# Kernel optimization log

Hardware: AMD Instinct MI355X
Metric: run time of the kernel (lower is better)

Reference implementation:

```python
import jax, jax.numpy as jnp
import numpy as np

L, T, D, H, NC = 4, 2, 128, 8, 7
DH = D // H
DFF = 4 * D
EPS = 1e-5


def _ln(x, w, b):
    m = jnp.mean(x, axis=-1, keepdims=True)
    v = jnp.mean((x - m) ** 2, axis=-1, keepdims=True)
    return (x - m) / jnp.sqrt(v + EPS) * w + b


def setup_inputs() -> dict:
    key = jax.random.key(0)
    ks = jax.random.split(key, 16)
    s = 0.02
    inp = {
        "x": jax.random.normal(ks[0], (65536, 1, 2 * D), dtype=jnp.float32),
        "token_proj_w": jax.random.normal(ks[1], (T * D, T * D), dtype=jnp.float32) * s,
        "token_proj_b": jnp.zeros((T * D,), jnp.float32),
        "pos_emb": jax.random.normal(ks[2], (1, T, D), dtype=jnp.float32),
        "qkv_w": jax.random.normal(ks[3], (L, 3 * D, D), dtype=jnp.float32) * s,
        "qkv_b": jnp.zeros((L, 3 * D), jnp.float32),
        "out_w": jax.random.normal(ks[4], (L, D, D), dtype=jnp.float32) * s,
        "out_b": jnp.zeros((L, D), jnp.float32),
        "ln1_w": jnp.ones((L, D), jnp.float32),
        "ln1_b": jnp.zeros((L, D), jnp.float32),
        "ff1_w": jax.random.normal(ks[5], (L, DFF, D), dtype=jnp.float32) * s,
        "ff1_b": jnp.zeros((L, DFF), jnp.float32),
        "ff2_w": jax.random.normal(ks[6], (L, D, DFF), dtype=jnp.float32) * s,
        "ff2_b": jnp.zeros((L, D), jnp.float32),
        "ln2_w": jnp.ones((L, D), jnp.float32),
        "ln2_b": jnp.zeros((L, D), jnp.float32),
        "lnf_w": jnp.ones((D,), jnp.float32),
        "lnf_b": jnp.zeros((D,), jnp.float32),
        "cls_ln_w": jnp.ones((D,), jnp.float32),
        "cls_ln_b": jnp.zeros((D,), jnp.float32),
        "cls_w": jax.random.normal(ks[7], (NC, D), dtype=jnp.float32) * s,
        "cls_b": jnp.zeros((NC,), jnp.float32),
    }
    return inp


def _forward(x, token_proj_w, token_proj_b, pos_emb, qkv_w, qkv_b, out_w, out_b,
             ln1_w, ln1_b, ff1_w, ff1_b, ff2_w, ff2_b, ln2_w, ln2_b,
             lnf_w, lnf_b, cls_ln_w, cls_ln_b, cls_w, cls_b):
    x = jnp.squeeze(x, 1)                                  # [B, 256]
    B = x.shape[0]
    tok = x @ token_proj_w.T + token_proj_b                # [B, 256]
    tok = tok.reshape(B, T, D) + pos_emb                   # [B, 2, 128]
    scale = 1.0 / jnp.sqrt(jnp.float32(DH))
    for i in range(L):
        # --- self-attention (post-norm, as in nn.TransformerEncoderLayer) ---
        qkv = jnp.einsum('btd,ed->bte', tok, qkv_w[i]) + qkv_b[i]   # [B,T,3D]
        q, k, v = jnp.split(qkv, 3, axis=-1)
        q = q.reshape(B, T, H, DH)
        k = k.reshape(B, T, H, DH)
        v = v.reshape(B, T, H, DH)
        scores = jnp.einsum('bqhd,bkhd->bhqk', q, k) * scale
        attn = jax.nn.softmax(scores, axis=-1)
        o = jnp.einsum('bhqk,bkhd->bqhd', attn, v).reshape(B, T, D)
        o = jnp.einsum('btd,ed->bte', o, out_w[i]) + out_b[i]
        tok = _ln(tok + o, ln1_w[i], ln1_b[i])
        # --- FFN ---
        h = jnp.einsum('btd,fd->btf', tok, ff1_w[i]) + ff1_b[i]
        h = jax.nn.gelu(h, approximate=False)
        h = jnp.einsum('btf,df->btd', h, ff2_w[i]) + ff2_b[i]
        tok = _ln(tok + h, ln2_w[i], ln2_b[i])
    tok = _ln(tok, lnf_w, lnf_b)                           # final encoder norm
    pooled = jnp.mean(tok, axis=1)                         # [B, D]
    out = _ln(pooled, cls_ln_w, cls_ln_b)
    out = jax.nn.gelu(out, approximate=False)
    return out @ cls_w.T + cls_b                           # [B, 7]


def reference(x, token_proj_w, token_proj_b, pos_emb, qkv_w, qkv_b, out_w, out_b,
              ln1_w, ln1_b, ff1_w, ff1_b, ff2_w, ff2_b, ln2_w, ln2_b,
              lnf_w, lnf_b, cls_ln_w, cls_ln_b, cls_w, cls_b):
    return _forward(x, token_proj_w, token_proj_b, pos_emb, qkv_w, qkv_b, out_w, out_b,
                    ln1_w, ln1_b, ff1_w, ff1_b, ff2_w, ff2_b, ln2_w, ln2_b,
                    lnf_w, lnf_b, cls_ln_w, cls_ln_b, cls_w, cls_b)
```

## Files before the change

kernel.cpp:

```cpp
#include <hip/hip_runtime.h>


#define DEV static __device__ __forceinline__

typedef __attribute__((ext_vector_type(8))) short short8;
typedef __attribute__((ext_vector_type(4))) float f32x4;

#define BS    32
#define MROWS 64
#define PITCH 136
#define XP    272
#define LEPS  1e-5f

#define OFF_TPW  0
#define OFF_QKVW 65536
#define OFF_OUTW 262144
#define OFF_FF1W 327680
#define OFF_FF2W 589824
#define WS_ELEMS 851968

DEV unsigned short f2b(float f) {
  unsigned u = __float_as_uint(f);
  return (unsigned short)((u + 0x7fffu + ((u >> 16) & 1u)) >> 16);
}
DEV float b2f(unsigned short s) { return __uint_as_float((unsigned)s << 16); }

DEV f32x4 MFMA(short8 a, short8 b, f32x4 c) {
  return __builtin_amdgcn_mfma_f32_16x16x32_bf16(a, b, c, 0, 0, 0);
}

DEV float gelu_f(float x) {
  float u = 0.7978845608028654f * (x + 0.044715f * x * x * x);
  float e = __expf(2.0f * u);
  float t = 1.0f - 2.0f / (e + 1.0f);
  return 0.5f * x * (1.0f + t);
}

DEV short8 ldfrag(const unsigned short* tile, int rowBase, int kk, int lane) {
  return *(const short8*)(tile + (rowBase + (lane & 15)) * PITCH + kk * 32 + (lane >> 4) * 8);
}
DEV short8 ldfragX(const unsigned short* tile, int rowBase, int koff, int lane) {
  return *(const short8*)(tile + (rowBase + (lane & 15)) * XP + koff + (lane >> 4) * 8);
}
DEV short8 ldBg(const unsigned short* __restrict__ base, int pitch, int colBase,
                int koff, int kk, int lane) {
  return *(const short8*)(base + (size_t)(colBase + (lane & 15)) * pitch +
                          koff + kk * 32 + (lane >> 4) * 8);
}

DEV void ln_residual_write(f32x4 (&val)[2][4], const float* __restrict__ w,
                           const float* __restrict__ b, unsigned short* sTok,
                           float* sRedP, float* sRedF, int tid) {
  const int wave = tid >> 6, lane = tid & 63, g = lane >> 4, j = lane & 15;
  float ps[4][4], pq[4][4];
#pragma unroll
  for (int rt = 0; rt < 4; ++rt)
#pragma unroll
    for (int r = 0; r < 4; ++r) {
      float v0 = val[0][rt][r], v1 = val[1][rt][r];
      float s = v0 + v1, q = v0 * v0 + v1 * v1;
#pragma unroll
      for (int m = 1; m < 16; m <<= 1) {
        s += __shfl_xor(s, m, 16);
        q += __shfl_xor(q, m, 16);
      }
      ps[rt][r] = s; pq[rt][r] = q;
    }
  if (j == 0) {
#pragma unroll
    for (int rt = 0; rt < 4; ++rt)
#pragma unroll
      for (int r = 0; r < 4; ++r) {
        int row = rt * 16 + g * 4 + r;
        sRedP[row * 8 + wave * 2]     = ps[rt][r];
        sRedP[row * 8 + wave * 2 + 1] = pq[rt][r];
      }
  }
  __syncthreads();
  if (tid < 64) {
    float s = 0.f, q = 0.f;
#pragma unroll
    for (int wv = 0; wv < 4; ++wv) {
      s += sRedP[tid * 8 + wv * 2];
      q += sRedP[tid * 8 + wv * 2 + 1];
    }
    float mean = s * (1.f / 128.f);
    sRedF[tid * 2]     = mean;
    sRedF[tid * 2 + 1] = rsqrtf(q * (1.f / 128.f) - mean * mean + LEPS);
  }
  __syncthreads();
#pragma unroll
  for (int h = 0; h < 2; ++h) {
    int n = (h * 4 + wave) * 16 + j;
    float wn = w[n], bn = b[n];
#pragma unroll
    for (int rt = 0; rt < 4; ++rt)
#pragma unroll
      for (int r = 0; r < 4; ++r) {
        int row = rt * 16 + g * 4 + r;
        float mean = sRedF[row * 2], rstd = sRedF[row * 2 + 1];
        sTok[row * PITCH + n] = f2b((val[h][rt][r] - mean) * rstd * wn + bn);
      }
  }
  __syncthreads();
}

__global__ __launch_bounds__(256)
void prep_w(const float* __restrict__ tpw, const float* __restrict__ qkvw,
            const float* __restrict__ outw, const float* __restrict__ ff1w,
            const float* __restrict__ ff2w, unsigned short* __restrict__ wsb) {
  int i = blockIdx.x * 256 + threadIdx.x;
  if (i >= WS_ELEMS) return;
  float v;
  if (i < OFF_QKVW)      v = tpw[i - OFF_TPW];
  else if (i < OFF_OUTW) v = qkvw[i - OFF_QKVW];
  else if (i < OFF_FF1W) v = outw[i - OFF_OUTW];
  else if (i < OFF_FF2W) v = ff1w[i - OFF_FF1W];
  else                   v = ff2w[i - OFF_FF2W];
  wsb[i] = f2b(v);
}

__global__ __launch_bounds__(256, 2)
void tx_fused(const float* __restrict__ x, const unsigned short* __restrict__ wsb,
              const float* __restrict__ tpb, const float* __restrict__ pos,
              const float* __restrict__ qkvb, const float* __restrict__ outb,
              const float* __restrict__ ln1w, const float* __restrict__ ln1b,
              const float* __restrict__ ff1b, const float* __restrict__ ff2b,
              const float* __restrict__ ln2w, const float* __restrict__ ln2b,
              const float* __restrict__ lnfw, const float* __restrict__ lnfb,
              const float* __restrict__ clnw, const float* __restrict__ clnb,
              const float* __restrict__ cw, const float* __restrict__ cb,
              float* __restrict__ out) {
  __shared__ __align__(16) unsigned short sTok[MROWS * PITCH];
  __shared__ __align__(16) unsigned short sStage[MROWS * PITCH];
  __shared__ float sRedP[MROWS * 8];
  __shared__ float sRedF[MROWS * 2];

  const int tid  = threadIdx.x;
  const int wave = tid >> 6;
  const int lane = tid & 63;
  const int g = lane >> 4, j = lane & 15;
  const size_t s0 = (size_t)blockIdx.x * BS;

  const unsigned short* tpwB  = wsb + OFF_TPW;
  const unsigned short* qkvwB = wsb + OFF_QKVW;
  const unsigned short* outwB = wsb + OFF_OUTW;
  const unsigned short* ff1wB = wsb + OFF_FF1W;
  const unsigned short* ff2wB = wsb + OFF_FF2W;

  const f32x4 zero4 = {0.f, 0.f, 0.f, 0.f};

  {
#pragma unroll
    for (int it = 0; it < 2; ++it) {
      int idx = it * 256 + tid;
      int r = idx >> 4, s = idx & 15;
      const float4* p = (const float4*)(x + (s0 + r) * 256 + s * 16);
      float4 f0 = p[0], f1 = p[1], f2 = p[2], f3 = p[3];
      short8 lo, hi;
      lo[0] = (short)f2b(f0.x); lo[1] = (short)f2b(f0.y);
      lo[2] = (short)f2b(f0.z); lo[3] = (short)f2b(f0.w);
      lo[4] = (short)f2b(f1.x); lo[5] = (short)f2b(f1.y);
      lo[6] = (short)f2b(f1.z); lo[7] = (short)f2b(f1.w);
      hi[0] = (short)f2b(f2.x); hi[1] = (short)f2b(f2.y);
      hi[2] = (short)f2b(f2.z); hi[3] = (short)f2b(f2.w);
      hi[4] = (short)f2b(f3.x); hi[5] = (short)f2b(f3.y);
      hi[6] = (short)f2b(f3.z); hi[7] = (short)f2b(f3.w);
      *(short8*)(sStage + r * XP + s * 16)     = lo;
      *(short8*)(sStage + r * XP + s * 16 + 8) = hi;
    }
  }
  __syncthreads();

  f32x4 accTP[2][2][2];
#pragma unroll
  for (int nc = 0; nc < 2; ++nc)
#pragma unroll
    for (int h = 0; h < 2; ++h)
#pragma unroll
      for (int rt = 0; rt < 2; ++rt) accTP[nc][h][rt] = zero4;

#pragma unroll
  for (int kc = 0; kc < 2; ++kc)
#pragma unroll
    for (int nc = 0; nc < 2; ++nc)
#pragma unroll
      for (int h = 0; h < 2; ++h) {
        int cb = nc * 128 + (h * 4 + wave) * 16;
        short8 bf[4];
#pragma unroll
        for (int kk = 0; kk < 4; ++kk)
          bf[kk] = ldBg(tpwB, 256, cb, kc * 128, kk, lane);
#pragma unroll
        for (int rt = 0; rt < 2; ++rt)
#pragma unroll
          for (int kk = 0; kk < 4; ++kk)
            accTP[nc][h][rt] = MFMA(ldfragX(sStage, rt * 16, kc * 128 + kk * 32, lane),
                                    bf[kk], accTP[nc][h][rt]);
      }
  __syncthreads();
#pragma unroll
  for (int nc = 0; nc < 2; ++nc)
#pragma unroll
    for (int h = 0; h < 2; ++h) {
      int d = (h * 4 + wave) * 16 + j;
      float bias = tpb[nc * 128 + d] + pos[nc * 128 + d];
#pragma unroll
      for (int rt = 0; rt < 2; ++rt)
#pragma unroll
        for (int r = 0; r < 4; ++r) {
          int sm = rt * 16 + g * 4 + r;
          sTok[(2 * sm + nc) * PITCH + d] = f2b(accTP[nc][h][rt][r] + bias);
        }
    }
  __syncthreads();

  for (int li = 0; li < 4; ++li) {
    const unsigned short* qkvL = qkvwB + (size_t)li * 49152;
    const unsigned short* outL = outwB + (size_t)li * 16384;
    const unsigned short* ff1L = ff1wB + (size_t)li * 65536;
    const unsigned short* ff2L = ff2wB + (size_t)li * 65536;

    short8 aT[4][4];
#pragma unroll
    for (int rt = 0; rt < 4; ++rt)
#pragma unroll
      for (int kk = 0; kk < 4; ++kk) aT[rt][kk] = ldfrag(sTok, rt * 16, kk, lane);

    f32x4 acc[6][4];
#pragma unroll
    for (int a = 0; a < 6; ++a)
#pragma unroll
      for (int rt = 0; rt < 4; ++rt) acc[a][rt] = zero4;

#pragma unroll
    for (int nc = 0; nc < 3; ++nc)
#pragma unroll
      for (int h = 0; h < 2; ++h) {
        int cb = nc * 128 + (h * 4 + wave) * 16;
        short8 bf[4];
#pragma unroll
        for (int kk = 0; kk < 4; ++kk) bf[kk] = ldBg(qkvL, 128, cb, 0, kk, lane);
        int a = nc * 2 + h;
#pragma unroll
        for (int rt = 0; rt < 4; ++rt)
#pragma unroll
          for (int kk = 0; kk < 4; ++kk)
            acc[a][rt] = MFMA(aT[rt][kk], bf[kk], acc[a][rt]);
      }
#pragma unroll
    for (int a = 0; a < 6; ++a) {
      int nc = a >> 1, h = a & 1;
      float bv = qkvb[li * 384 + nc * 128 + (h * 4 + wave) * 16 + j];
#pragma unroll
      for (int rt = 0; rt < 4; ++rt) acc[a][rt] += bv;
    }

#pragma unroll
    for (int hh = 0; hh < 2; ++hh) {
      int head = hh * 4 + wave;
#pragma unroll
      for (int rt = 0; rt < 4; ++rt)
#pragma unroll
        for (int sp = 0; sp < 2; ++sp) {
          int r0 = sp * 2, r1 = r0 + 1;
          float q0 = acc[hh][rt][r0],     q1 = acc[hh][rt][r1];
          float k0 = acc[2 + hh][rt][r0], k1 = acc[2 + hh][rt][r1];
          float s00 = q0 * k0, s01 = q0 * k1, s10 = q1 * k0, s11 = q1 * k1;
#pragma unroll
          for (int m = 1; m < 16; m <<= 1) {
            s00 += __shfl_xor(s00, m, 16);
            s01 += __shfl_xor(s01, m, 16);
            s10 += __shfl_xor(s10, m, 16);
            s11 += __shfl_xor(s11, m, 16);
          }
          s00 *= 0.25f; s01 *= 0.25f; s10 *= 0.25f; s11 *= 0.25f;
          float m0 = fmaxf(s00, s01), m1 = fmaxf(s10, s11);
          float e00 = __expf(s00 - m0), e01 = __expf(s01 - m0);
          float e10 = __expf(s10 - m1), e11 = __expf(s11 - m1);
          float i0 = 1.f / (e00 + e01), i1 = 1.f / (e10 + e11);
          float v0 = acc[4 + hh][rt][r0], v1 = acc[4 + hh][rt][r1];
          float o0 = (e00 * v0 + e01 * v1) * i0;
          float o1 = (e10 * v0 + e11 * v1) * i1;
          int rowb = rt * 16 + g * 4 + r0;
          int col  = head * 16 + j;
          sStage[rowb * PITCH + col]       = f2b(o0);
          sStage[(rowb + 1) * PITCH + col] = f2b(o1);
        }
    }
    __syncthreads();

    short8 aO[4][4];
#pragma unroll
    for (int rt = 0; rt < 4; ++rt)
#pragma unroll
      for (int kk = 0; kk < 4; ++kk) aO[rt][kk] = ldfrag(sStage, rt * 16, kk, lane);

    f32x4 accO[2][4];
#pragma unroll
    for (int h = 0; h < 2; ++h)
#pragma unroll
      for (int rt = 0; rt < 4; ++rt) accO[h][rt] = zero4;
#pragma unroll
    for (int h = 0; h < 2; ++h) {
      int cb = (h * 4 + wave) * 16;
      short8 bf[4];
#pragma unroll
      for (int kk = 0; kk < 4; ++kk) bf[kk] = ldBg(outL, 128, cb, 0, kk, lane);
#pragma unroll
      for (int rt = 0; rt < 4; ++rt)
#pragma unroll
        for (int kk = 0; kk < 4; ++kk)
          accO[h][rt] = MFMA(aO[rt][kk], bf[kk], accO[h][rt]);
    }
#pragma unroll
    for (int h = 0; h < 2; ++h) {
      int n = (h * 4 + wave) * 16 + j;
      float ob = outb[li * 128 + n];
#pragma unroll
      for (int rt = 0; rt < 4; ++rt)
#pragma unroll
        for (int r = 0; r < 4; ++r) {
          int row = rt * 16 + g * 4 + r;
          accO[h][rt][r] += ob + b2f(sTok[row * PITCH + n]);
        }
    }
    ln_residual_write(accO, ln1w + li * 128, ln1b + li * 128, sTok, sRedP, sRedF, tid);

    short8 aF[4][4];
#pragma unroll
    for (int rt = 0; rt < 4; ++rt)
#pragma unroll
      for (int kk = 0; kk < 4; ++kk) aF[rt][kk] = ldfrag(sTok, rt * 16, kk, lane);

    f32x4 accF[2][4];
#pragma unroll
    for (int h = 0; h < 2; ++h)
#pragma unroll
      for (int rt = 0; rt < 4; ++rt) accF[h][rt] = zero4;

    for (int fc = 0; fc < 4; ++fc) {
      f32x4 hacc[2][4];
#pragma unroll
      for (int h = 0; h < 2; ++h)
#pragma unroll
        for (int rt = 0; rt < 4; ++rt) hacc[h][rt] = zero4;
#pragma unroll
      for (int h = 0; h < 2; ++h) {
        int cb = fc * 128 + (h * 4 + wave) * 16;
        short8 bf[4];
#pragma unroll
        for (int kk = 0; kk < 4; ++kk) bf[kk] = ldBg(ff1L, 128, cb, 0, kk, lane);
#pragma unroll
        for (int rt = 0; rt < 4; ++rt)
#pragma unroll
          for (int kk = 0; kk < 4; ++kk)
            hacc[h][rt] = MFMA(aF[rt][kk], bf[kk], hacc[h][rt]);
      }
      __syncthreads();
#pragma unroll
      for (int h = 0; h < 2; ++h) {
        int nl = (h * 4 + wave) * 16 + j;
        float bb = ff1b[li * 512 + fc * 128 + nl];
#pragma unroll
        for (int rt = 0; rt < 4; ++rt)
#pragma unroll
          for (int r = 0; r < 4; ++r) {
            float hv = gelu_f(hacc[h][rt][r] + bb);
            sStage[(rt * 16 + g * 4 + r) * PITCH + nl] = f2b(hv);
          }
      }
      __syncthreads();
      short8 aH[4][4];
#pragma unroll
      for (int rt = 0; rt < 4; ++rt)
#pragma unroll
        for (int kk = 0; kk < 4; ++kk) aH[rt][kk] = ldfrag(sStage, rt * 16, kk, lane);
#pragma unroll
      for (int h = 0; h < 2; ++h) {
        int cb = (h * 4 + wave) * 16;
        short8 bf[4];
#pragma unroll
        for (int kk = 0; kk < 4; ++kk)
          bf[kk] = ldBg(ff2L, 512, cb, fc * 128, kk, lane);
#pragma unroll
        for (int rt = 0; rt < 4; ++rt)
#pragma unroll
          for (int kk = 0; kk < 4; ++kk)
            accF[h][rt] = MFMA(aH[rt][kk], bf[kk], accF[h][rt]);
      }
    }
#pragma unroll
    for (int h = 0; h < 2; ++h) {
      int n = (h * 4 + wave) * 16 + j;
      float fb = ff2b[li * 128 + n];
#pragma unroll
      for (int rt = 0; rt < 4; ++rt)
#pragma unroll
        for (int r = 0; r < 4; ++r) {
          int row = rt * 16 + g * 4 + r;
          accF[h][rt][r] += fb + b2f(sTok[row * PITCH + n]);
        }
    }
    ln_residual_write(accF, ln2w + li * 128, ln2b + li * 128, sTok, sRedP, sRedF, tid);
  }

  {
    int row = tid >> 2, q4 = tid & 3;
    const unsigned short* rp = sTok + row * PITCH + q4 * 32;
    float vb[32];
    float s = 0.f, sq = 0.f;
#pragma unroll
    for (int t8 = 0; t8 < 4; ++t8) {
      short8 v = *(const short8*)(rp + t8 * 8);
#pragma unroll
      for (int e = 0; e < 8; ++e) {
        float f = b2f((unsigned short)v[e]);
        vb[t8 * 8 + e] = f; s += f; sq += f * f;
      }
    }
    s  += __shfl_xor(s, 1, 4);  s  += __shfl_xor(s, 2, 4);
    sq += __shfl_xor(sq, 1, 4); sq += __shfl_xor(sq, 2, 4);
    float mean = s * (1.f / 128.f);
    float rstd = rsqrtf(sq * (1.f / 128.f) - mean * mean + LEPS);
    unsigned short* wp = sTok + row * PITCH + q4 * 32;
#pragma unroll
    for (int c = 0; c < 32; ++c) {
      int col = q4 * 32 + c;
      wp[c] = f2b((vb[c] - mean) * rstd * lnfw[col] + lnfb[col]);
    }
  }
  __syncthreads();
  {
    int sIdx = tid >> 3, oct = tid & 7;
    float pv[16];
    float s = 0.f, sq = 0.f;
#pragma unroll
    for (int t8 = 0; t8 < 2; ++t8) {
      short8 va  = *(const short8*)(sTok + (2 * sIdx) * PITCH + oct * 16 + t8 * 8);
      short8 vb2 = *(const short8*)(sTok + (2 * sIdx + 1) * PITCH + oct * 16 + t8 * 8);
#pragma unroll
      for (int e = 0; e < 8; ++e) {
        float f = 0.5f * (b2f((unsigned short)va[e]) + b2f((unsigned short)vb2[e]));
        pv[t8 * 8 + e] = f; s += f; sq += f * f;
      }
    }
    s  += __shfl_xor(s, 1, 8);  s  += __shfl_xor(s, 2, 8);  s  += __shfl_xor(s, 4, 8);
    sq += __shfl_xor(sq, 1, 8); sq += __shfl_xor(sq, 2, 8); sq += __shfl_xor(sq, 4, 8);
    float mean = s * (1.f / 128.f);
    float rstd = rsqrtf(sq * (1.f / 128.f) - mean * mean + LEPS);
    float gv[16];
#pragma unroll
    for (int c = 0; c < 16; ++c) {
      int col = oct * 16 + c;
      gv[c] = gelu_f((pv[c] - mean) * rstd * clnw[col] + clnb[col]);
    }
#pragma unroll
    for (int cc = 0; cc < 7; ++cc) {
      float p = 0.f;
#pragma unroll
      for (int c = 0; c < 16; ++c) p += gv[c] * cw[cc * 128 + oct * 16 + c];
      p += __shfl_xor(p, 1, 8); p += __shfl_xor(p, 2, 8); p += __shfl_xor(p, 4, 8);
      if (oct == 0) out[(s0 + sIdx) * 7 + cc] = p + cb[cc];
    }
  }
}

extern "C" void kernel_launch(void* const* d_in, const int* in_sizes, int n_in,
                              void* d_out, int out_size, void* d_ws, size_t ws_size,
                              hipStream_t stream) {
  (void)n_in; (void)out_size; (void)ws_size;
  const float* x    = (const float*)d_in[0];
  const float* tpw  = (const float*)d_in[1];
  const float* tpb  = (const float*)d_in[2];
  const float* pos  = (const float*)d_in[3];
  const float* qkvw = (const float*)d_in[4];
  const float* qkvb = (const float*)d_in[5];
  const float* outw = (const float*)d_in[6];
  const float* outb = (const float*)d_in[7];
  const float* ln1w = (const float*)d_in[8];
  const float* ln1b = (const float*)d_in[9];
  const float* ff1w = (const float*)d_in[10];
  const float* ff1b = (const float*)d_in[11];
  const float* ff2w = (const float*)d_in[12];
  const float* ff2b = (const float*)d_in[13];
  const float* ln2w = (const float*)d_in[14];
  const float* ln2b = (const float*)d_in[15];
  const float* lnfw = (const float*)d_in[16];
  const float* lnfb = (const float*)d_in[17];
  const float* clnw = (const float*)d_in[18];
  const float* clnb = (const float*)d_in[19];
  const float* cw   = (const float*)d_in[20];
  const float* cb   = (const float*)d_in[21];
  unsigned short* wsb = (unsigned short*)d_ws;

  int B = in_sizes[0] / 256;

  hipLaunchKernelGGL(prep_w, dim3((WS_ELEMS + 255) / 256), dim3(256), 0, stream,
                     tpw, qkvw, outw, ff1w, ff2w, wsb);
  hipLaunchKernelGGL(tx_fused, dim3(B / BS), dim3(256), 0, stream,
                     x, wsb, tpb, pos, qkvb, outb, ln1w, ln1b, ff1b, ff2b,
                     ln2w, ln2b, lnfw, lnfb, clnw, clnb, cw, cb, (float*)d_out);
}
```

Measured before the change: 719.3 us.

## Prefetch next-stage weight fragments into LDS with async global-to-LDS loads

Adds a per-wave LDS prefetch buffer and uses global_load_lds to fetch the weight fragments of the next GEMM stage (the first QKV slice, out-proj, the first FF1 chunk, FF2 chunks, and the next layer's QKV) while the current stage computes. Each stage then waits on vmcnt and reads its B fragments from LDS instead of issuing blocking global loads right before the MFMAs. This is meant to hide global/L2 weight-load latency. In exchange it adds 32KB of LDS per block, which pressures the two-blocks-per-CU occupancy target. The full vmcnt(0) waits can also serialize against other outstanding loads, and reuse of the buffer relies on ordering between the LDS reads and the next async writes.

```diff
diff --git a/kernel.cpp b/kernel.cpp
--- a/kernel.cpp
+++ b/kernel.cpp
@@ -47,6 +47,27 @@
   return *(const short8*)(base + (size_t)(colBase + (lane & 15)) * pitch +
                           koff + kk * 32 + (lane >> 4) * 8);
 }
+
+DEV void pf_issue(unsigned short* sPF, int wave, int lane,
+                  const unsigned short* __restrict__ base, int pitch,
+                  int ncoff, int koff) {
+#pragma unroll
+  for (int h = 0; h < 2; ++h)
+#pragma unroll
+    for (int kk = 0; kk < 4; ++kk) {
+      int cb = ncoff + (h * 4 + wave) * 16;
+      const unsigned short* src = base + (size_t)(cb + (lane & 15)) * pitch +
+                                  koff + kk * 32 + (lane >> 4) * 8;
+      __builtin_amdgcn_global_load_lds(
+          (const __attribute__((address_space(1))) void*)src,
+          (__attribute__((address_space(3))) void*)(sPF + wave * 4096 + (h * 4 + kk) * 512),
+          16, 0, 0);
+    }
+}
+DEV short8 pf_read(const unsigned short* sPF, int wave, int h, int kk, int lane) {
+  return *(const short8*)(sPF + wave * 4096 + (h * 4 + kk) * 512 + lane * 8);
+}
+#define PF_WAIT() asm volatile("s_waitcnt vmcnt(0)" ::: "memory")
 
 DEV void ln_residual_write(f32x4 (&val)[2][4], const float* __restrict__ w,
                            const float* __restrict__ b, unsigned short* sTok,
@@ -133,6 +154,7 @@
               float* __restrict__ out) {
   __shared__ __align__(16) unsigned short sTok[MROWS * PITCH];
   __shared__ __align__(16) unsigned short sStage[MROWS * PITCH];
+  __shared__ __align__(16) unsigned short sPF[4 * 4096];
   __shared__ float sRedP[MROWS * 8];
   __shared__ float sRedF[MROWS * 2];
 
@@ -172,6 +194,8 @@
   }
   __syncthreads();
 
+  pf_issue(sPF, wave, lane, qkvwB, 128, 0, 0);
+
   f32x4 accTP[2][2][2];
 #pragma unroll
   for (int nc = 0; nc < 2; ++nc)
@@ -233,8 +257,22 @@
 #pragma unroll
       for (int rt = 0; rt < 4; ++rt) acc[a][rt] = zero4;
 
-#pragma unroll
-    for (int nc = 0; nc < 3; ++nc)
+    PF_WAIT();
+    short8 bq[2][4];
+#pragma unroll
+    for (int h = 0; h < 2; ++h)
+#pragma unroll
+      for (int kk = 0; kk < 4; ++kk) bq[h][kk] = pf_read(sPF, wave, h, kk, lane);
+    pf_issue(sPF, wave, lane, outL, 128, 0, 0);
+#pragma unroll
+    for (int h = 0; h < 2; ++h)
+#pragma unroll
+      for (int rt = 0; rt < 4; ++rt)
+#pragma unroll
+        for (int kk = 0; kk < 4; ++kk)
+          acc[h][rt] = MFMA(aT[rt][kk], bq[h][kk], acc[h][rt]);
+#pragma unroll
+    for (int nc = 1; nc < 3; ++nc)
 #pragma unroll
       for (int h = 0; h < 2; ++h) {
         int cb = nc * 128 + (h * 4 + wave) * 16;
@@ -296,23 +334,26 @@
 #pragma unroll
       for (int kk = 0; kk < 4; ++kk) aO[rt][kk] = ldfrag(sStage, rt * 16, kk, lane);
 
+    PF_WAIT();
+    short8 bo[2][4];
+#pragma unroll
+    for (int h = 0; h < 2; ++h)
+#pragma unroll
+      for (int kk = 0; kk < 4; ++kk) bo[h][kk] = pf_read(sPF, wave, h, kk, lane);
+    pf_issue(sPF, wave, lane, ff1L, 128, 0, 0);
+
     f32x4 accO[2][4];
 #pragma unroll
     for (int h = 0; h < 2; ++h)
 #pragma unroll
       for (int rt = 0; rt < 4; ++rt) accO[h][rt] = zero4;
 #pragma unroll
-    for (int h = 0; h < 2; ++h) {
-      int cb = (h * 4 + wave) * 16;
-      short8 bf[4];
-#pragma unroll
-      for (int kk = 0; kk < 4; ++kk) bf[kk] = ldBg(outL, 128, cb, 0, kk, lane);
+    for (int h = 0; h < 2; ++h)
 #pragma unroll
       for (int rt = 0; rt < 4; ++rt)
 #pragma unroll
         for (int kk = 0; kk < 4; ++kk)
-          accO[h][rt] = MFMA(aO[rt][kk], bf[kk], accO[h][rt]);
-    }
+          accO[h][rt] = MFMA(aO[rt][kk], bo[h][kk], accO[h][rt]);
 #pragma unroll
     for (int h = 0; h < 2; ++h) {
       int n = (h * 4 + wave) * 16 + j;
@@ -345,17 +386,35 @@
       for (int h = 0; h < 2; ++h)
 #pragma unroll
         for (int rt = 0; rt < 4; ++rt) hacc[h][rt] = zero4;
-#pragma unroll
-      for (int h = 0; h < 2; ++h) {
-        int cb = fc * 128 + (h * 4 + wave) * 16;
-        short8 bf[4];
-#pragma unroll
-        for (int kk = 0; kk < 4; ++kk) bf[kk] = ldBg(ff1L, 128, cb, 0, kk, lane);
-#pragma unroll
-        for (int rt = 0; rt < 4; ++rt)
-#pragma unroll
-          for (int kk = 0; kk < 4; ++kk)
-            hacc[h][rt] = MFMA(aF[rt][kk], bf[kk], hacc[h][rt]);
+
+      if (fc == 0) {
+        PF_WAIT();
+        short8 b1[2][4];
+#pragma unroll
+        for (int h = 0; h < 2; ++h)
+#pragma unroll
+          for (int kk = 0; kk < 4; ++kk) b1[h][kk] = pf_read(sPF, wave, h, kk, lane);
+        pf_issue(sPF, wave, lane, ff2L, 512, 0, 0);
+#pragma unroll
+        for (int h = 0; h < 2; ++h)
+#pragma unroll
+          for (int rt = 0; rt < 4; ++rt)
+#pragma unroll
+            for (int kk = 0; kk < 4; ++kk)
+              hacc[h][rt] = MFMA(aF[rt][kk], b1[h][kk], hacc[h][rt]);
+      } else {
+#pragma unroll
+        for (int h = 0; h < 2; ++h) {
+          int cb = fc * 128 + (h * 4 + wave) * 16;
+          short8 bf[4];
+#pragma unroll
+          for (int kk = 0; kk < 4; ++kk) bf[kk] = ldBg(ff1L, 128, cb, 0, kk, lane);
+#pragma unroll
+          for (int rt = 0; rt < 4; ++rt)
+#pragma unroll
+            for (int kk = 0; kk < 4; ++kk)
+              hacc[h][rt] = MFMA(aF[rt][kk], bf[kk], hacc[h][rt]);
+        }
       }
       __syncthreads();
 #pragma unroll
@@ -376,19 +435,22 @@
       for (int rt = 0; rt < 4; ++rt)
 #pragma unroll
         for (int kk = 0; kk < 4; ++kk) aH[rt][kk] = ldfrag(sStage, rt * 16, kk, lane);
-#pragma unroll
-      for (int h = 0; h < 2; ++h) {
-        int cb = (h * 4 + wave) * 16;
-        short8 bf[4];
-#pragma unroll
-        for (int kk = 0; kk < 4; ++kk)
-          bf[kk] = ldBg(ff2L, 512, cb, fc * 128, kk, lane);
+
+      PF_WAIT();
+      short8 b2[2][4];
+#pragma unroll
+      for (int h = 0; h < 2; ++h)
+#pragma unroll
+        for (int kk = 0; kk < 4; ++kk) b2[h][kk] = pf_read(sPF, wave, h, kk, lane);
+      if (fc < 3)      pf_issue(sPF, wave, lane, ff2L, 512, 0, (fc + 1) * 128);
+      else if (li < 3) pf_issue(sPF, wave, lane, qkvL + 49152, 128, 0, 0);
+#pragma unroll
+      for (int h = 0; h < 2; ++h)
 #pragma unroll
         for (int rt = 0; rt < 4; ++rt)
 #pragma unroll
           for (int kk = 0; kk < 4; ++kk)
-            accF[h][rt] = MFMA(aH[rt][kk], bf[kk], accF[h][rt]);
-      }
+            accF[h][rt] = MFMA(aH[rt][kk], b2[h][kk], accF[h][rt]);
     }
 #pragma unroll
     for (int h = 0; h < 2; ++h) {
```

Result: slower. 946.0 us (+31.5%).
